# Optimization experiments

Measured on AMD Instinct MI355X. Metric: run time of the kernel, lower is better.

The kernel has to match this reference:

```python
import jax, jax.numpy as jnp
import numpy as np

EMBED_DIM = 1024
NHEAD = 16
HEAD_DIM = EMBED_DIM // NHEAD  # 64
B, S = 2, 2048


def _rotate_half(x):
    x1, x2 = jnp.split(x, 2, axis=-1)
    return jnp.concatenate([-x2, x1], axis=-1)


def _apply_rope(t, cos, sin):
    # t: (B, H, S, Dh); cos/sin: (S, Dh) broadcast over leading dims
    return t * cos + _rotate_half(t) * sin


def setup_inputs() -> dict:
    key = jax.random.key(0)
    ks = jax.random.split(key, 6)
    x = jax.random.normal(ks[0], (B, S, EMBED_DIM), dtype=jnp.float32)
    # real RoPE tables: theta_i = 10000^(-2i/Dh), duplicated for the two halves
    inv_freq = 1.0 / (10000.0 ** (jnp.arange(0, HEAD_DIM, 2, dtype=jnp.float32) / HEAD_DIM))
    freqs = jnp.outer(jnp.arange(S, dtype=jnp.float32), inv_freq)  # (S, Dh/2)
    emb = jnp.concatenate([freqs, freqs], axis=-1)  # (S, Dh)
    cos = jnp.cos(emb)
    sin = jnp.sin(emb)
    W_in = jax.random.normal(ks[1], (EMBED_DIM, 3 * EMBED_DIM), dtype=jnp.float32) * 0.02
    b_in = jax.random.normal(ks[2], (3 * EMBED_DIM,), dtype=jnp.float32) * 0.02
    W_out = jax.random.normal(ks[3], (EMBED_DIM, EMBED_DIM), dtype=jnp.float32) * 0.02
    b_out = jax.random.normal(ks[4], (EMBED_DIM,), dtype=jnp.float32) * 0.02
    return {"x": x, "cos": cos, "sin": sin, "W_in": W_in, "b_in": b_in,
            "W_out": W_out, "b_out": b_out}


def reference(x, cos, sin, W_in, b_in, W_out, b_out):
    Bs, Ss, D = x.shape
    qkv = x @ W_in + b_in  # (B, S, 3D)
    q, k, v = jnp.split(qkv, 3, axis=-1)
    # (B, S, D) -> (B, H, S, Dh)
    def heads(t):
        return t.reshape(Bs, Ss, NHEAD, HEAD_DIM).transpose(0, 2, 1, 3)
    q, k, v = heads(q), heads(k), heads(v)
    q = _apply_rope(q, cos, sin)
    k = _apply_rope(k, cos, sin)
    scale = 1.0 / jnp.sqrt(jnp.array(HEAD_DIM, dtype=x.dtype))
    scores = jnp.einsum('bhqd,bhkd->bhqk', q, k) * scale
    attn = jax.nn.softmax(scores, axis=-1)
    out = jnp.einsum('bhqk,bhkd->bhqd', attn, v)
    out = out.transpose(0, 2, 1, 3).reshape(Bs, Ss, D)
    return out @ W_out + b_out
```

## Files before the change

kernel.cpp:

```cpp
#include <hip/hip_runtime.h>
#include <hip/hip_bf16.h>

typedef float f32x4 __attribute__((ext_vector_type(4)));
typedef short s16x8 __attribute__((ext_vector_type(8)));

typedef const __attribute__((address_space(1))) unsigned int* as1u;
typedef __attribute__((address_space(3))) unsigned int* as3u;

__device__ __forceinline__ unsigned short f2bf(float f) {
    union { float f; unsigned u; } v; v.f = f;
    unsigned u = v.u;
    u += 0x7fffu + ((u >> 16) & 1u);
    return (unsigned short)(u >> 16);
}

__device__ __forceinline__ void gload16(const void* g, void* l3) {
    __builtin_amdgcn_global_load_lds((as1u)g, (as3u)l3, 16, 0, 0);
}

__device__ __forceinline__ int swzo(int row, int cb) {
    return row * 128 + (cb ^ ((row & 7) << 4));
}

#define LOG2E 1.4426950408889634f
#define QSCALE (0.125f * LOG2E)

__global__ __launch_bounds__(256) void prep_kernel(
    const float* __restrict__ x, unsigned short* __restrict__ xb,
    const float* __restrict__ W_in, unsigned short* __restrict__ Wt_in,
    const float* __restrict__ W_out, unsigned short* __restrict__ Wot)
{
    const int t = threadIdx.x;
    int blk = blockIdx.x;
    if (blk < 2048) {
        size_t i = ((size_t)blk * 256 + t) * 8;
        float4 a = *(const float4*)&x[i];
        float4 b = *(const float4*)&x[i + 4];
        s16x8 p;
        p[0] = (short)f2bf(a.x); p[1] = (short)f2bf(a.y);
        p[2] = (short)f2bf(a.z); p[3] = (short)f2bf(a.w);
        p[4] = (short)f2bf(b.x); p[5] = (short)f2bf(b.y);
        p[6] = (short)f2bf(b.z); p[7] = (short)f2bf(b.w);
        *(s16x8*)&xb[i] = p;
        return;
    }
    const float* W;
    unsigned short* Wt;
    int N;
    if (blk < 2816) { blk -= 2048; W = W_in;  Wt = Wt_in; N = 3072; }
    else            { blk -= 2816; W = W_out; Wt = Wot;   N = 1024; }
    __shared__ alignas(16) short T[64 * 64];
    const int KB = 16;
    const int kb = blk % KB, nb = blk / KB;
#pragma unroll
    for (int pass = 0; pass < 4; ++pass) {
        int k = pass * 16 + (t >> 4);
        int n4 = (t & 15) * 4;
        float4 v = *(const float4*)&W[(size_t)(kb * 64 + k) * N + nb * 64 + n4];
        short4 s4;
        s4.x = (short)f2bf(v.x); s4.y = (short)f2bf(v.y);
        s4.z = (short)f2bf(v.z); s4.w = (short)f2bf(v.w);
        *(short4*)((char*)T + k * 128 + ((n4 * 2) ^ ((k & 7) << 4))) = s4;
    }
    __syncthreads();
#pragma unroll
    for (int pass = 0; pass < 4; ++pass) {
        int n = pass * 16 + (t >> 4);
        int k4 = (t & 15) * 4;
        short4 s4;
        s4.x = *(const short*)((const char*)T + (k4 + 0) * 128 + ((n * 2) ^ (((k4 + 0) & 7) << 4)));
        s4.y = *(const short*)((const char*)T + (k4 + 1) * 128 + ((n * 2) ^ (((k4 + 1) & 7) << 4)));
        s4.z = *(const short*)((const char*)T + (k4 + 2) * 128 + ((n * 2) ^ (((k4 + 2) & 7) << 4)));
        s4.w = *(const short*)((const char*)T + (k4 + 3) * 128 + ((n * 2) ^ (((k4 + 3) & 7) << 4)));
        *(short4*)&Wt[(size_t)(nb * 64 + n) * 1024 + kb * 64 + k4] = s4;
    }
}

__global__ __launch_bounds__(256) void qkv_rope_kernel(
    const unsigned short* __restrict__ xb, const unsigned short* __restrict__ Wt,
    const float* __restrict__ bias, const float* __restrict__ cosb,
    const float* __restrict__ sinb,
    unsigned short* __restrict__ Qb, unsigned short* __restrict__ Kb,
    unsigned short* __restrict__ Vb)
{
    __shared__ alignas(16) short As[128 * 64];
    __shared__ alignas(16) short Bs[128 * 64];
    const int bid = blockIdx.x;
    const int xcd = bid & 7, ii = bid >> 3;
    const int mb = (xcd & 3) * 8 + (ii & 7);
    const int nb = (xcd >> 2) * 12 + (ii >> 3);
    const int t = threadIdx.x, w = t >> 6, l = t & 63;
    const int g = l >> 4, j = l & 15;
    const int wm = w >> 1, wn = w & 1;
    const int m0 = mb * 128, n0 = nb * 128;

    f32x4 acc[4][4];
#pragma unroll
    for (int mi = 0; mi < 4; ++mi)
#pragma unroll
        for (int ni = 0; ni < 4; ++ni) acc[mi][ni] = (f32x4){0.f, 0.f, 0.f, 0.f};

    for (int kt = 0; kt < 1024; kt += 64) {
#pragma unroll
        for (int i = 0; i < 4; ++i) {
            int pos = (w * 4 + i) * 1024 + l * 16;
            int r = pos >> 7;
            int lb = (pos & 127) ^ ((r & 7) << 4);
            gload16(&Wt[(size_t)(n0 + r) * 1024 + kt + (lb >> 1)],
                    (char*)Bs + (w * 4 + i) * 1024);
            gload16(&xb[(size_t)(m0 + r) * 1024 + kt + (lb >> 1)],
                    (char*)As + (w * 4 + i) * 1024);
        }
        __syncthreads();
#pragma unroll
        for (int kf = 0; kf < 2; ++kf) {
            s16x8 af[4], bv[4];
#pragma unroll
            for (int mi = 0; mi < 4; ++mi)
                af[mi] = *(const s16x8*)((const char*)As + swzo(wm * 64 + mi * 16 + j, kf * 64 + g * 16));
#pragma unroll
            for (int ni = 0; ni < 4; ++ni)
                bv[ni] = *(const s16x8*)((const char*)Bs + swzo(wn * 64 + ni * 16 + j, kf * 64 + g * 16));
#pragma unroll
            for (int mi = 0; mi < 4; ++mi)
#pragma unroll
                for (int ni = 0; ni < 4; ++ni)
                    acc[mi][ni] = __builtin_amdgcn_mfma_f32_16x16x32_bf16(af[mi], bv[ni], acc[mi][ni], 0, 0, 0);
        }
        __syncthreads();
    }

    const int row0 = m0 + wm * 64;
    const int col0 = n0 + wn * 64;
    const int sec = col0 >> 10;
    const int h = (col0 & 1023) >> 6;

    if (sec < 2) {
        unsigned short* dst = (sec == 0) ? Qb : Kb;
        const float qs = (sec == 0) ? QSCALE : 1.0f;
#pragma unroll
        for (int nt = 0; nt < 2; ++nt) {
            const int d = nt * 16 + j;
            const float b1 = bias[col0 + d];
            const float b2 = bias[col0 + d + 32];
#pragma unroll
            for (int mi = 0; mi < 4; ++mi) {
#pragma unroll
                for (int r = 0; r < 4; ++r) {
                    int row = row0 + mi * 16 + g * 4 + r;
                    int s = row & 2047, bb = row >> 11;
                    float c = cosb[s * 64 + d], sn = sinb[s * 64 + d];
                    float x1 = acc[mi][nt][r] + b1;
                    float x2 = acc[mi][nt + 2][r] + b2;
                    float lo = (x1 * c - x2 * sn) * qs;
                    float hi = (x1 * sn + x2 * c) * qs;
                    size_t base = ((size_t)(bb * 16 + h) * 2048 + s) * 64;
                    dst[base + d] = f2bf(lo);
                    dst[base + d + 32] = f2bf(hi);
                }
            }
        }
    } else {
#pragma unroll
        for (int nt = 0; nt < 4; ++nt) {
            const int d = nt * 16 + j;
            const float bvv = bias[col0 + d];
#pragma unroll
            for (int mi = 0; mi < 4; ++mi) {
#pragma unroll
                for (int r = 0; r < 4; ++r) {
                    int row = row0 + mi * 16 + g * 4 + r;
                    int s = row & 2047, bb = row >> 11;
                    size_t base = ((size_t)(bb * 16 + h) * 2048 + s) * 64;
                    Vb[base + d] = f2bf(acc[mi][nt][r] + bvv);
                }
            }
        }
    }
}

#define NROUND 16
__global__ __launch_bounds__(512, 4) void attn_kernel(
    const unsigned short* __restrict__ Qb, const unsigned short* __restrict__ Kb,
    const unsigned short* __restrict__ Vb, unsigned short* __restrict__ AO)
{
    __shared__ alignas(16) short Ks[2][2 * 64 * 64];
    __shared__ alignas(16) short Vt[2][2 * 64 * 64];
    const int bid = blockIdx.x;
    const int bh = (bid & 7) + ((bid >> 7) << 3);
    const int qt = (bid >> 3) & 15;
    const int t = threadIdx.x, w = t >> 6, l = t & 63;
    const int g = l >> 4, j = l & 15;
    const unsigned short* Qh = Qb + (size_t)bh * 131072;
    const unsigned short* Kh = Kb + (size_t)bh * 131072;
    const unsigned short* Vh = Vb + (size_t)bh * 131072;
    const int q0 = qt * 128 + w * 16;

    s16x8 aq[2];
    aq[0] = *(const s16x8*)&Qh[(size_t)(q0 + j) * 64 + g * 8];
    aq[1] = *(const s16x8*)&Qh[(size_t)(q0 + j) * 64 + 32 + g * 8];

    float lt_ = 0.f;
    f32x4 o[4];
#pragma unroll
    for (int dt = 0; dt < 4; ++dt) o[dt] = (f32x4){0.f, 0.f, 0.f, 0.f};

    const bool vrole = (w < 4);
    const int tv = t & 255;
    const int vk = (tv & 31) * 2;
    const int vd = (tv >> 5) * 8;
    const int kw = (w & 3);

    s16x8 va[2], vb2[2];

    if (vrole) {
#pragma unroll
        for (int s = 0; s < 2; ++s) {
            va[s]  = *(const s16x8*)&Vh[(size_t)(s * 64 + vk) * 64 + vd];
            vb2[s] = *(const s16x8*)&Vh[(size_t)(s * 64 + vk + 1) * 64 + vd];
        }
    } else {
#pragma unroll
        for (int i = 0; i < 4; ++i) {
            int p = (kw * 4 + i) * 1024 + l * 16;
            int s = p >> 13, q = p & 8191;
            int r = q >> 7, lb = (q & 127) ^ ((r & 7) << 4);
            gload16(&Kh[(size_t)(s * 64 + r) * 64 + (lb >> 1)],
                    (char*)Ks[0] + (kw * 4 + i) * 1024);
        }
    }
    asm volatile("s_waitcnt vmcnt(0)" ::: "memory");
    if (vrole) {
#pragma unroll
        for (int s = 0; s < 2; ++s)
#pragma unroll
            for (int dd = 0; dd < 8; ++dd) {
                int d = vd + dd;
                unsigned pkv = (unsigned)(unsigned short)va[s][dd] | ((unsigned)(unsigned short)vb2[s][dd] << 16);
                *(unsigned*)((char*)Vt[0] + s * 8192 + d * 128 + ((vk * 2) ^ ((d & 7) << 4))) = pkv;
            }
    }
    asm volatile("s_waitcnt lgkmcnt(0)" ::: "memory");
    __builtin_amdgcn_s_barrier();

    for (int rr = 0; rr < NROUND; ++rr) {
        const int cur = rr & 1, nxt = cur ^ 1;
        const int kvp = ((rr + 1) & (NROUND - 1)) * 128;

        if (vrole) {
#pragma unroll
            for (int s = 0; s < 2; ++s) {
                va[s]  = *(const s16x8*)&Vh[(size_t)(kvp + s * 64 + vk) * 64 + vd];
                vb2[s] = *(const s16x8*)&Vh[(size_t)(kvp + s * 64 + vk + 1) * 64 + vd];
            }
        } else {
#pragma unroll
            for (int i = 0; i < 4; ++i) {
                int p = (kw * 4 + i) * 1024 + l * 16;
                int s = p >> 13, q = p & 8191;
                int r = q >> 7, lb = (q & 127) ^ ((r & 7) << 4);
                gload16(&Kh[(size_t)(kvp + s * 64 + r) * 64 + (lb >> 1)],
                        (char*)Ks[nxt] + (kw * 4 + i) * 1024);
            }
        }

        f32x4 sc[2][4];
#pragma unroll
        for (int sub = 0; sub < 2; ++sub)
#pragma unroll
            for (int nt = 0; nt < 4; ++nt) sc[sub][nt] = (f32x4){0.f, 0.f, 0.f, 0.f};
        __builtin_amdgcn_s_setprio(1);
#pragma unroll
        for (int sub = 0; sub < 2; ++sub) {
            const char* kbase = (const char*)Ks[cur] + sub * 8192;
#pragma unroll
            for (int kf = 0; kf < 2; ++kf) {
                s16x8 bk[4];
#pragma unroll
                for (int nt = 0; nt < 4; ++nt)
                    bk[nt] = *(const s16x8*)(kbase + swzo(nt * 16 + j, kf * 64 + g * 16));
#pragma unroll
                for (int nt = 0; nt < 4; ++nt)
                    sc[sub][nt] = __builtin_amdgcn_mfma_f32_16x16x32_bf16(bk[nt], aq[kf], sc[sub][nt], 0, 0, 0);
            }
        }
        __builtin_amdgcn_s_setprio(0);

#pragma unroll
        for (int sub = 0; sub < 2; ++sub) {
            const char* vbase = (const char*)Vt[cur] + sub * 8192;

            float rs = 0.f;
#pragma unroll
            for (int nt = 0; nt < 4; ++nt)
#pragma unroll
                for (int r = 0; r < 4; ++r) {
                    sc[sub][nt][r] = __builtin_amdgcn_exp2f(sc[sub][nt][r]);
                    rs += sc[sub][nt][r];
                }
            lt_ += rs;

            unsigned pk[4][2];
#pragma unroll
            for (int nt = 0; nt < 4; ++nt)
#pragma unroll
                for (int s = 0; s < 2; ++s)
                    asm("v_cvt_pk_bf16_f32 %0, %1, %2"
                        : "=v"(pk[nt][s]) : "v"(sc[sub][nt][2 * s]), "v"(sc[sub][nt][2 * s + 1]));

#pragma unroll
            for (int kf = 0; kf < 2; ++kf) {
                unsigned A0 = pk[2 * kf][0], A1 = pk[2 * kf][1];
                unsigned B0 = pk[2 * kf + 1][0], B1 = pk[2 * kf + 1][1];
                asm("v_permlane32_swap_b32 %0, %1" : "+v"(A0), "+v"(B0));
                asm("v_permlane32_swap_b32 %0, %1" : "+v"(A1), "+v"(B1));
                asm("v_permlane16_swap_b32 %0, %1" : "+v"(A0), "+v"(B0));
                asm("v_permlane16_swap_b32 %0, %1" : "+v"(A1), "+v"(B1));
                union { unsigned u[4]; s16x8 v; } fr;
                fr.u[0] = A0;
                fr.u[1] = A1;
                fr.u[2] = B0;
                fr.u[3] = B1;
                __builtin_amdgcn_s_setprio(1);
#pragma unroll
                for (int dt = 0; dt < 4; ++dt) {
                    s16x8 vb = *(const s16x8*)(vbase + swzo(dt * 16 + j, kf * 64 + g * 16));
                    o[dt] = __builtin_amdgcn_mfma_f32_16x16x32_bf16(fr.v, vb, o[dt], 0, 0, 0);
                }
                __builtin_amdgcn_s_setprio(0);
            }
        }

        if (vrole) {
#pragma unroll
            for (int s = 0; s < 2; ++s)
#pragma unroll
                for (int dd = 0; dd < 8; ++dd) {
                    int d = vd + dd;
                    unsigned pkv = (unsigned)(unsigned short)va[s][dd] | ((unsigned)(unsigned short)vb2[s][dd] << 16);
                    *(unsigned*)((char*)Vt[nxt] + s * 8192 + d * 128 + ((vk * 2) ^ ((d & 7) << 4))) = pkv;
                }
        }
        asm volatile("s_waitcnt vmcnt(0) lgkmcnt(0)" ::: "memory");
        __builtin_amdgcn_s_barrier();
    }

    lt_ += __shfl_xor(lt_, 16);
    lt_ += __shfl_xor(lt_, 32);

    const int b = bh >> 4, h = bh & 15;
#pragma unroll
    for (int r = 0; r < 4; ++r) {
        float inv = 1.0f / __shfl(lt_, g * 4 + r);
        int s = q0 + g * 4 + r;
        size_t base = ((size_t)b * 2048 + s) * 1024 + h * 64;
#pragma unroll
        for (int dt = 0; dt < 4; ++dt)
            AO[base + dt * 16 + j] = f2bf(o[dt][r] * inv);
    }
}

__global__ __launch_bounds__(256) void out_gemm_kernel(
    const unsigned short* __restrict__ A, const unsigned short* __restrict__ Wot,
    const float* __restrict__ bias, float* __restrict__ out)
{
    __shared__ alignas(16) short As[128 * 64];
    __shared__ alignas(16) short Bs[128 * 64];
    const int bid = blockIdx.x;
    const int xcd = bid & 7, ii = bid >> 3;
    const int mb = (xcd & 3) * 8 + (ii & 7);
    const int nb = (xcd >> 2) * 4 + (ii >> 3);
    const int t = threadIdx.x, w = t >> 6, l = t & 63;
    const int g = l >> 4, j = l & 15;
    const int wm = w >> 1, wn = w & 1;
    const int m0 = mb * 128, n0 = nb * 128;

    f32x4 acc[4][4];
#pragma unroll
    for (int mi = 0; mi < 4; ++mi)
#pragma unroll
        for (int ni = 0; ni < 4; ++ni) acc[mi][ni] = (f32x4){0.f, 0.f, 0.f, 0.f};

    for (int kt = 0; kt < 1024; kt += 64) {
#pragma unroll
        for (int i = 0; i < 4; ++i) {
            int pos = (w * 4 + i) * 1024 + l * 16;
            int r = pos >> 7;
            int lb = (pos & 127) ^ ((r & 7) << 4);
            gload16(&A[(size_t)(m0 + r) * 1024 + kt + (lb >> 1)],
                    (char*)As + (w * 4 + i) * 1024);
            gload16(&Wot[(size_t)(n0 + r) * 1024 + kt + (lb >> 1)],
                    (char*)Bs + (w * 4 + i) * 1024);
        }
        __syncthreads();
#pragma unroll
        for (int kf = 0; kf < 2; ++kf) {
            s16x8 af[4], bv[4];
#pragma unroll
            for (int mi = 0; mi < 4; ++mi)
                af[mi] = *(const s16x8*)((const char*)As + swzo(wm * 64 + mi * 16 + j, kf * 64 + g * 16));
#pragma unroll
            for (int ni = 0; ni < 4; ++ni)
                bv[ni] = *(const s16x8*)((const char*)Bs + swzo(wn * 64 + ni * 16 + j, kf * 64 + g * 16));
#pragma unroll
            for (int mi = 0; mi < 4; ++mi)
#pragma unroll
                for (int ni = 0; ni < 4; ++ni)
                    acc[mi][ni] = __builtin_amdgcn_mfma_f32_16x16x32_bf16(af[mi], bv[ni], acc[mi][ni], 0, 0, 0);
        }
        __syncthreads();
    }

    const int row0 = m0 + wm * 64;
    const int col0 = n0 + wn * 64;
#pragma unroll
    for (int ni = 0; ni < 4; ++ni) {
        const int col = col0 + ni * 16 + j;
        const float bvv = bias[col];
#pragma unroll
        for (int mi = 0; mi < 4; ++mi)
#pragma unroll
            for (int r = 0; r < 4; ++r) {
                int row = row0 + mi * 16 + g * 4 + r;
                out[(size_t)row * 1024 + col] = acc[mi][ni][r] + bvv;
            }
    }
}

extern "C" void kernel_launch(void* const* d_in, const int* in_sizes, int n_in,
                              void* d_out, int out_size, void* d_ws, size_t ws_size,
                              hipStream_t stream) {
    const float* x     = (const float*)d_in[0];
    const float* cosb  = (const float*)d_in[1];
    const float* sinb  = (const float*)d_in[2];
    const float* W_in  = (const float*)d_in[3];
    const float* b_in  = (const float*)d_in[4];
    const float* W_out = (const float*)d_in[5];
    const float* b_out = (const float*)d_in[6];
    float* out = (float*)d_out;

    const size_t HBUF = 2ull * 16 * 2048 * 64;
    if (ws_size < (4 * HBUF + 1024 * 1024) * sizeof(unsigned short)) return;
    unsigned short* Qb = (unsigned short*)d_ws;
    unsigned short* Kb = Qb + HBUF;
    unsigned short* Vb = Kb + HBUF;
    unsigned short* R  = Vb + HBUF;
    unsigned short* Wt_in = R;
    unsigned short* AO    = R;
    unsigned short* Wot   = R + HBUF;
    unsigned short* xbuf  = (unsigned short*)d_out;

    hipLaunchKernelGGL(prep_kernel, dim3(3072), dim3(256), 0, stream,
                       x, xbuf, W_in, Wt_in, W_out, Wot);
    hipLaunchKernelGGL(qkv_rope_kernel, dim3(768), dim3(256), 0, stream,
                       xbuf, Wt_in, b_in, cosb, sinb, Qb, Kb, Vb);
    hipLaunchKernelGGL(attn_kernel, dim3(512), dim3(512), 0, stream,
                       Qb, Kb, Vb, AO);
    hipLaunchKernelGGL(out_gemm_kernel, dim3(256), dim3(256), 0, stream,
                       AO, Wot, b_out, out);
}
```

Measured before the change: 122.7 us.

## Double-buffer QKV GEMM with 256x256 tiles and 512-thread blocks

Rewrites the QKV+RoPE GEMM main loop to prefetch the next K-slice into a second LDS buffer while MFMAs run on the current one. It uses explicit vmcnt waits and raw barriers in place of two __syncthreads per iteration. Tiles grow from 128x128 to 256x256, with 8 waves each computing a 128x64 sub-tile, and MFMA sections are wrapped in s_setprio. This cuts grid size from 768 to 192 blocks and uses 128KB LDS per block, so fewer blocks than CUs run, trading occupancy and parallelism for more data reuse and latency hiding. The XCD-aware block remap is dropped.

```diff
diff --git a/kernel.cpp b/kernel.cpp
--- a/kernel.cpp
+++ b/kernel.cpp
@@ -76,61 +76,77 @@
     }
 }
 
-__global__ __launch_bounds__(256) void qkv_rope_kernel(
+__global__ __launch_bounds__(512, 2) void qkv_rope_kernel(
     const unsigned short* __restrict__ xb, const unsigned short* __restrict__ Wt,
     const float* __restrict__ bias, const float* __restrict__ cosb,
     const float* __restrict__ sinb,
     unsigned short* __restrict__ Qb, unsigned short* __restrict__ Kb,
     unsigned short* __restrict__ Vb)
 {
-    __shared__ alignas(16) short As[128 * 64];
-    __shared__ alignas(16) short Bs[128 * 64];
+    __shared__ alignas(16) short As[2][256 * 64];
+    __shared__ alignas(16) short Bs[2][256 * 64];
     const int bid = blockIdx.x;
-    const int xcd = bid & 7, ii = bid >> 3;
-    const int mb = (xcd & 3) * 8 + (ii & 7);
-    const int nb = (xcd >> 2) * 12 + (ii >> 3);
+    const int mb = bid & 15, nb = bid >> 4;
     const int t = threadIdx.x, w = t >> 6, l = t & 63;
     const int g = l >> 4, j = l & 15;
-    const int wm = w >> 1, wn = w & 1;
-    const int m0 = mb * 128, n0 = nb * 128;
-
-    f32x4 acc[4][4];
-#pragma unroll
-    for (int mi = 0; mi < 4; ++mi)
+    const int wm = w >> 2, wn = w & 3;
+    const int m0 = mb * 256, n0 = nb * 256;
+
+    f32x4 acc[8][4];
+#pragma unroll
+    for (int mi = 0; mi < 8; ++mi)
 #pragma unroll
         for (int ni = 0; ni < 4; ++ni) acc[mi][ni] = (f32x4){0.f, 0.f, 0.f, 0.f};
 
-    for (int kt = 0; kt < 1024; kt += 64) {
+#pragma unroll
+    for (int i = 0; i < 4; ++i) {
+        int p = (w * 4 + i) * 1024 + l * 16;
+        int r = p >> 7, lb = (p & 127) ^ ((r & 7) << 4);
+        gload16(&xb[(size_t)(m0 + r) * 1024 + (lb >> 1)], (char*)As[0] + (w * 4 + i) * 1024);
+        gload16(&Wt[(size_t)(n0 + r) * 1024 + (lb >> 1)], (char*)Bs[0] + (w * 4 + i) * 1024);
+    }
+    asm volatile("s_waitcnt vmcnt(0)" ::: "memory");
+    __builtin_amdgcn_s_barrier();
+
+    for (int kti = 0; kti < 16; ++kti) {
+        const int cur = kti & 1, nxt = cur ^ 1;
+        const int ktn = ((kti + 1) & 15) * 64;
+
 #pragma unroll
         for (int i = 0; i < 4; ++i) {
-            int pos = (w * 4 + i) * 1024 + l * 16;
-            int r = pos >> 7;
-            int lb = (pos & 127) ^ ((r & 7) << 4);
-            gload16(&Wt[(size_t)(n0 + r) * 1024 + kt + (lb >> 1)],
-                    (char*)Bs + (w * 4 + i) * 1024);
-            gload16(&xb[(size_t)(m0 + r) * 1024 + kt + (lb >> 1)],
-                    (char*)As + (w * 4 + i) * 1024);
-        }
-        __syncthreads();
+            int p = (w * 4 + i) * 1024 + l * 16;
+            int r = p >> 7, lb = (p & 127) ^ ((r & 7) << 4);
+            gload16(&xb[(size_t)(m0 + r) * 1024 + ktn + (lb >> 1)], (char*)As[nxt] + (w * 4 + i) * 1024);
+            gload16(&Wt[(size_t)(n0 + r) * 1024 + ktn + (lb >> 1)], (char*)Bs[nxt] + (w * 4 + i) * 1024);
+        }
+        asm volatile("s_waitcnt vmcnt(8)" ::: "memory");
+        __builtin_amdgcn_s_barrier();
+
 #pragma unroll
         for (int kf = 0; kf < 2; ++kf) {
-            s16x8 af[4], bv[4];
-#pragma unroll
-            for (int mi = 0; mi < 4; ++mi)
-                af[mi] = *(const s16x8*)((const char*)As + swzo(wm * 64 + mi * 16 + j, kf * 64 + g * 16));
+            s16x8 bv[4];
 #pragma unroll
             for (int ni = 0; ni < 4; ++ni)
-                bv[ni] = *(const s16x8*)((const char*)Bs + swzo(wn * 64 + ni * 16 + j, kf * 64 + g * 16));
-#pragma unroll
-            for (int mi = 0; mi < 4; ++mi)
-#pragma unroll
-                for (int ni = 0; ni < 4; ++ni)
-                    acc[mi][ni] = __builtin_amdgcn_mfma_f32_16x16x32_bf16(af[mi], bv[ni], acc[mi][ni], 0, 0, 0);
-        }
-        __syncthreads();
-    }
-
-    const int row0 = m0 + wm * 64;
+                bv[ni] = *(const s16x8*)((const char*)Bs[cur] + swzo(wn * 64 + ni * 16 + j, kf * 64 + g * 16));
+#pragma unroll
+            for (int mh = 0; mh < 2; ++mh) {
+                s16x8 af[4];
+#pragma unroll
+                for (int mi = 0; mi < 4; ++mi)
+                    af[mi] = *(const s16x8*)((const char*)As[cur] + swzo(wm * 128 + mh * 64 + mi * 16 + j, kf * 64 + g * 16));
+                __builtin_amdgcn_s_setprio(1);
+#pragma unroll
+                for (int mi = 0; mi < 4; ++mi)
+#pragma unroll
+                    for (int ni = 0; ni < 4; ++ni)
+                        acc[mh * 4 + mi][ni] = __builtin_amdgcn_mfma_f32_16x16x32_bf16(af[mi], bv[ni], acc[mh * 4 + mi][ni], 0, 0, 0);
+                __builtin_amdgcn_s_setprio(0);
+            }
+        }
+        __builtin_amdgcn_s_barrier();
+    }
+
+    const int row0 = m0 + wm * 128;
     const int col0 = n0 + wn * 64;
     const int sec = col0 >> 10;
     const int h = (col0 & 1023) >> 6;
@@ -144,7 +160,7 @@
             const float b1 = bias[col0 + d];
             const float b2 = bias[col0 + d + 32];
 #pragma unroll
-            for (int mi = 0; mi < 4; ++mi) {
+            for (int mi = 0; mi < 8; ++mi) {
 #pragma unroll
                 for (int r = 0; r < 4; ++r) {
                     int row = row0 + mi * 16 + g * 4 + r;
@@ -166,7 +182,7 @@
             const int d = nt * 16 + j;
             const float bvv = bias[col0 + d];
 #pragma unroll
-            for (int mi = 0; mi < 4; ++mi) {
+            for (int mi = 0; mi < 8; ++mi) {
 #pragma unroll
                 for (int r = 0; r < 4; ++r) {
                     int row = row0 + mi * 16 + g * 4 + r;
@@ -452,7 +468,7 @@
 
     hipLaunchKernelGGL(prep_kernel, dim3(3072), dim3(256), 0, stream,
                        x, xbuf, W_in, Wt_in, W_out, Wot);
-    hipLaunchKernelGGL(qkv_rope_kernel, dim3(768), dim3(256), 0, stream,
+    hipLaunchKernelGGL(qkv_rope_kernel, dim3(192), dim3(512), 0, stream,
                        xbuf, Wt_in, b_in, cosb, sinb, Qb, Kb, Vb);
     hipLaunchKernelGGL(attn_kernel, dim3(512), dim3(512), 0, stream,
                        Qb, Kb, Vb, AO);
```

New measurement: 119.8 us. 1.02x faster.
